# Kernel tuning notes

Hardware: AMD Instinct MI355X
Metric: run time of the kernel (lower is better)

Reference implementation:

```python
import jax, jax.numpy as jnp
import numpy as np

INPUT_DIM = 256
OUTPUT_DIM = 256
COND_DIM = 128
HIDDEN = 128
BATCH = 512


def setup_inputs() -> dict:
    key = jax.random.key(0)
    ks = jax.random.split(key, 8)
    IO = INPUT_DIM * OUTPUT_DIM
    x = jax.random.normal(ks[0], (BATCH, INPUT_DIM), dtype=jnp.float32)
    cond = jax.random.normal(ks[1], (BATCH, COND_DIM), dtype=jnp.float32)
    base_weight = jax.random.normal(ks[2], (INPUT_DIM, OUTPUT_DIM), dtype=jnp.float32) * 0.01
    base_bias = jnp.zeros((OUTPUT_DIM,), dtype=jnp.float32)
    # hypernet: Linear(cond_dim, hidden) -> ReLU -> Linear(hidden, I*O + O)
    w1 = jax.random.normal(ks[3], (COND_DIM, HIDDEN), dtype=jnp.float32) * (1.0 / np.sqrt(COND_DIM))
    b1 = jnp.zeros((HIDDEN,), dtype=jnp.float32)
    w2 = jax.random.normal(ks[4], (HIDDEN, IO + OUTPUT_DIM), dtype=jnp.float32) * (1.0 / np.sqrt(HIDDEN))
    b2 = jnp.zeros((IO + OUTPUT_DIM,), dtype=jnp.float32)
    return {"x": x, "cond": cond, "base_weight": base_weight, "base_bias": base_bias,
            "w1": w1, "b1": b1, "w2": w2, "b2": b2}


def reference(x, cond, base_weight, base_bias, w1, b1, w2, b2):
    B = x.shape[0]
    IO = INPUT_DIM * OUTPUT_DIM
    # hypernet MLP producing per-sample weight/bias deltas
    h = jax.nn.relu(cond @ w1 + b1)                      # [B, hidden]
    dyn = h @ w2 + b2                                    # [B, I*O + O]
    weight_delta = dyn[:, :IO].reshape(B, INPUT_DIM, OUTPUT_DIM)
    bias_delta = dyn[:, IO:]                             # [B, O]
    W = base_weight[None, :, :] + weight_delta           # [B, I, O]
    b = base_bias[None, :] + bias_delta                  # [B, O]
    out = jnp.einsum('bi,bio->bo', x, W) + b             # per-sample GEMV
    return out
```

## Files before the change

### kernel.cpp

```cpp
#include <hip/hip_runtime.h>
#include <hip/hip_bf16.h>
#include <stdint.h>

#define BATCH    512
#define IN_DIM   256
#define OUT_DIM  256
#define COND_DIM 128
#define HIDDEN   128
#define W2_COLS  65792
#define H_STRIDE 132
#define PLANE_SZ 65536
#define NCHUNKS  18
#define OUT_ELEMS (BATCH * OUT_DIM)
#define SLICE_OFF ((size_t)131 * PLANE_SZ)

typedef __attribute__((ext_vector_type(8))) short bf16x8;
typedef __attribute__((ext_vector_type(4))) float f32x4;

__device__ float          g_h[BATCH * H_STRIDE + 8];
__device__ unsigned short g_hbf[BATCH * HIDDEN];
__device__ unsigned short g_xbf[BATCH * IN_DIM];

static __device__ __forceinline__ unsigned short f2bf(float f) {
    union { float f; unsigned int u; } v; v.f = f;
    unsigned int r = v.u + 0x7FFFu + ((v.u >> 16) & 1u);
    return (unsigned short)(r >> 16);
}
static __device__ __forceinline__ unsigned int pack2(float a, float b) {
    return (unsigned int)f2bf(a) | ((unsigned int)f2bf(b) << 16);
}
static __device__ __forceinline__ float bf2f(unsigned short u) {
    union { unsigned int u; float f; } v; v.u = ((unsigned int)u) << 16;
    return v.f;
}

template<int N>
static __device__ __forceinline__ void wait_vmcnt() {
    if constexpr (N == 0)      asm volatile("s_waitcnt vmcnt(0)" ::: "memory");
    else if constexpr (N == 2) asm volatile("s_waitcnt vmcnt(2)" ::: "memory");
    else                       asm volatile("s_waitcnt vmcnt(4)" ::: "memory");
}

__global__ __launch_bounds__(256)
void hyper_prep_kernel(const float* __restrict__ x,
                       const float* __restrict__ cond,
                       const float* __restrict__ base_weight,
                       const float* __restrict__ w1,
                       const float* __restrict__ b1,
                       const float* __restrict__ w2,
                       const float* __restrict__ b2,
                       unsigned short* __restrict__ wt) {
    const int bx = blockIdx.x;
    const int t  = threadIdx.x;
    if (bx < 2088) {
        int p, it, ot; const float* src; int rstride;
        if (bx < 2080) {
            p = bx >> 4; int sub = bx & 15; it = sub >> 2; ot = sub & 3;
            src = (p < 128) ? (w2 + (size_t)p * W2_COLS) : (p == 128 ? b2 : base_weight);
            rstride = OUT_DIM;
        } else {
            p = 130; int sub = bx - 2080; it = sub >> 2; ot = sub & 3;
            src = w2 + 65536; rstride = W2_COLS;
        }
        int o  = ot * 64 + (t & 63);
        int i0 = it * 64 + (t >> 6) * 16;
        unsigned int vv[8];
        #pragma unroll
        for (int r = 0; r < 8; ++r) {
            float a = src[(size_t)(i0 + 2 * r)     * rstride + o];
            float b = src[(size_t)(i0 + 2 * r + 1) * rstride + o];
            vv[r] = pack2(a, b);
        }
        unsigned int* dst = (unsigned int*)(wt + (size_t)p * PLANE_SZ + (size_t)o * 256 + i0);
        *(uint4*)dst       = *(uint4*)&vv[0];
        *(uint4*)(dst + 4) = *(uint4*)&vv[4];
    } else if (bx < 2104) {
        int base = (bx - 2088) * 8192 + t * 32;
        #pragma unroll
        for (int g = 0; g < 4; ++g) {
            const float4* s4 = (const float4*)(x + base + g * 8);
            float4 a = s4[0], b = s4[1];
            unsigned int vv[4] = { pack2(a.x, a.y), pack2(a.z, a.w),
                                   pack2(b.x, b.y), pack2(b.z, b.w) };
            *(uint4*)(g_xbf + base + g * 8) = *(uint4*)vv;
        }
    } else {
        __shared__ float c[2][COND_DIM];
        int bb = t >> 7, k = t & 127;
        int b  = (bx - 2104) * 2 + bb;
        c[bb][k] = cond[b * COND_DIM + k];
        __syncthreads();
        float acc = b1[k];
        #pragma unroll 8
        for (int i = 0; i < COND_DIM; ++i)
            acc += c[bb][i] * w1[i * HIDDEN + k];
        acc = fmaxf(acc, 0.0f);
        g_h[b * H_STRIDE + k] = acc;
        g_hbf[b * HIDDEN + k] = f2bf(acc);
        if (k < 4) g_h[b * H_STRIDE + 128 + k] = 1.0f;
    }
}

template<int NSLABS>
static __device__ __forceinline__ void run_gemm(
    int nplanes, int p0, const unsigned short* asrc, int astride,
    const unsigned short* __restrict__ wt, unsigned short* __restrict__ slices,
    int chunk, int b0, int o0, int t,
    unsigned short (*B_lds)[64 * 64], const float* h_s)
{
    constexpr int LOG2S = (NSLABS == 4) ? 2 : 1;
    const int lane = t & 63, wave = t >> 6;
    const int wm = wave >> 1, wn = wave & 1;
    const int qg = lane >> 4, ncol = lane & 15;

    const int drow = lane >> 3;
    const int dcol = ((lane & 7) ^ drow) * 8;
    const int nsteps = nplanes * NSLABS;

    auto dmaB = [&](int s) {
        const int plane = p0 + (s >> LOG2S);
        const int i0    = (s & (NSLABS - 1)) * 64;
        const int buf   = s & 3;
        const unsigned short* gp = wt + (size_t)plane * PLANE_SZ
            + (size_t)(o0 + wave * 16 + drow) * 256 + i0 + dcol;
        __builtin_amdgcn_global_load_lds(
            (const __attribute__((address_space(1))) unsigned int*)gp,
            (__attribute__((address_space(3))) unsigned int*)&B_lds[buf][wave * 16 * 64],
            16, 0, 0);
        __builtin_amdgcn_global_load_lds(
            (const __attribute__((address_space(1))) unsigned int*)(gp + 8 * 256),
            (__attribute__((address_space(3))) unsigned int*)&B_lds[buf][(wave * 16 + 8) * 64],
            16, 0, 0);
    };

    bf16x8 xf[NSLABS][2][2];
    #pragma unroll
    for (int sl = 0; sl < NSLABS; ++sl)
        #pragma unroll
        for (int ks = 0; ks < 2; ++ks)
            #pragma unroll
            for (int mf = 0; mf < 2; ++mf)
                xf[sl][ks][mf] = *(const bf16x8*)(asrc
                    + (size_t)(b0 + wm * 32 + mf * 16 + ncol) * astride
                    + sl * 64 + ks * 32 + qg * 8);

    f32x4 acc[2][2] = {};
    f32x4 pacc[2][2];
    float hv[2][4];

    dmaB(0); dmaB(1);
    if (nsteps > 2) dmaB(2);

    for (int pl = 0; pl < nplanes; ++pl) {
        #pragma unroll
        for (int sl = 0; sl < NSLABS; ++sl) {
            const int s = pl * NSLABS + sl;

            if (s <= nsteps - 3)      wait_vmcnt<4>();
            else if (s == nsteps - 2) wait_vmcnt<2>();
            else                      wait_vmcnt<0>();
            __builtin_amdgcn_s_barrier();
            asm volatile("" ::: "memory");

            if (sl == 0) {
                #pragma unroll
                for (int mf = 0; mf < 2; ++mf)
                    #pragma unroll
                    for (int r = 0; r < 4; ++r)
                        hv[mf][r] = h_s[(wm * 32 + mf * 16 + qg * 4 + r) * 8 + pl];
                #pragma unroll
                for (int a = 0; a < 2; ++a)
                    #pragma unroll
                    for (int bq = 0; bq < 2; ++bq)
                        pacc[a][bq] = (f32x4){0.f, 0.f, 0.f, 0.f};
            }

            const int buf = s & 3;
            #pragma unroll
            for (int ks = 0; ks < 2; ++ks) {
                bf16x8 bfr[2];
                #pragma unroll
                for (int nf = 0; nf < 2; ++nf) {
                    int n = wn * 32 + nf * 16 + ncol;
                    bfr[nf] = *(const bf16x8*)&B_lds[buf][(n * 8 + ((ks * 4 + qg) ^ (n & 7))) * 8];
                }
                #pragma unroll
                for (int mf = 0; mf < 2; ++mf)
                    #pragma unroll
                    for (int nf = 0; nf < 2; ++nf)
                        pacc[mf][nf] = __builtin_amdgcn_mfma_f32_16x16x32_bf16(
                            xf[sl][ks][mf], bfr[nf], pacc[mf][nf], 0, 0, 0);
            }

            if (sl == NSLABS - 1) {
                #pragma unroll
                for (int mf = 0; mf < 2; ++mf)
                    #pragma unroll
                    for (int nf = 0; nf < 2; ++nf)
                        #pragma unroll
                        for (int r = 0; r < 4; ++r)
                            acc[mf][nf][r] += hv[mf][r] * pacc[mf][nf][r];
            }

            if (s + 3 < nsteps) dmaB(s + 3);
        }
    }

    unsigned short* slice = slices + (size_t)chunk * OUT_ELEMS;
    #pragma unroll
    for (int mf = 0; mf < 2; ++mf)
        #pragma unroll
        for (int nf = 0; nf < 2; ++nf)
            #pragma unroll
            for (int r = 0; r < 4; ++r) {
                int row = b0 + wm * 32 + mf * 16 + qg * 4 + r;
                int col = o0 + wn * 32 + nf * 16 + ncol;
                slice[(size_t)row * OUT_DIM + col] = f2bf(acc[mf][nf][r]);
            }
}

__global__ __launch_bounds__(256, 3)
void hyper_main_kernel(const unsigned short* __restrict__ wt,
                       unsigned short* __restrict__ slices) {
    __shared__ __align__(16) unsigned short B_lds[4][64 * 64];
    __shared__ float h_s[512];

    const int bx    = blockIdx.x;
    const int chunk = bx >> 5;
    const int rem   = bx & 31;
    const int b0    = (rem >> 2) * 64;
    const int o0    = (rem & 3) * 64;
    const int t     = threadIdx.x;

    const int p0 = (chunk < 16) ? chunk * 8 : (chunk == 16 ? 128 : 130);

    h_s[t]       = g_h[(b0      + (t >> 3)) * H_STRIDE + p0 + (t & 7)];
    h_s[256 + t] = g_h[(b0 + 32 + (t >> 3)) * H_STRIDE + p0 + (t & 7)];
    __syncthreads();

    if (chunk < 17)
        run_gemm<4>(chunk < 16 ? 8 : 2, p0, g_xbf, IN_DIM,
                    wt, slices, chunk, b0, o0, t, B_lds, h_s);
    else
        run_gemm<2>(1, p0, g_hbf, HIDDEN,
                    wt, slices, chunk, b0, o0, t, B_lds, h_s);
}

__global__ void hyper_reduce_kernel(const unsigned short* __restrict__ slices,
                                    const float* __restrict__ base_bias,
                                    const float* __restrict__ b2,
                                    float* __restrict__ out) {
    int i = blockIdx.x * 256 + threadIdx.x;
    int o = (i & 63) * 4;
    float4 bb = *(const float4*)(base_bias + o);
    float4 c2 = *(const float4*)(b2 + 65536 + o);
    float4 a;
    a.x = bb.x + c2.x; a.y = bb.y + c2.y; a.z = bb.z + c2.z; a.w = bb.w + c2.w;
    #pragma unroll
    for (int c = 0; c < NCHUNKS; ++c) {
        ushort4 v = *(const ushort4*)(slices + (size_t)c * OUT_ELEMS + (size_t)i * 4);
        a.x += bf2f(v.x); a.y += bf2f(v.y); a.z += bf2f(v.z); a.w += bf2f(v.w);
    }
    ((float4*)out)[i] = a;
}

extern "C" void kernel_launch(void* const* d_in, const int* in_sizes, int n_in,
                              void* d_out, int out_size, void* d_ws, size_t ws_size,
                              hipStream_t stream) {
    const float* x           = (const float*)d_in[0];
    const float* cond        = (const float*)d_in[1];
    const float* base_weight = (const float*)d_in[2];
    const float* base_bias   = (const float*)d_in[3];
    const float* w1          = (const float*)d_in[4];
    const float* b1          = (const float*)d_in[5];
    const float* w2          = (const float*)d_in[6];
    const float* b2          = (const float*)d_in[7];
    float* out = (float*)d_out;
    unsigned short* ws = (unsigned short*)d_ws;

    hyper_prep_kernel<<<2360, 256, 0, stream>>>(x, cond, base_weight, w1, b1, w2, b2, ws);
    hyper_main_kernel<<<NCHUNKS * 32, 256, 0, stream>>>(ws, ws + SLICE_OFF);
    hyper_reduce_kernel<<<OUT_ELEMS / 4 / 256, 256, 0, stream>>>(ws + SLICE_OFF, base_bias, b2, out);
}
```

Baseline: 120.1 us.

## Replace slice buffers and reduce kernel with atomic adds into output

Each main-kernel tile now atomically adds its fp32 partial sum straight into the output instead of writing a bf16 slice per chunk. The bias initialisation moves into extra blocks of the prep kernel, and the separate reduce kernel is removed. This drops one launch and the slice write/read traffic, and it also removes the bf16 rounding of partial sums. In exchange, 18 chunks contend through scattered scalar atomics, and the summation order is no longer deterministic.

```diff
diff --git a/kernel.cpp b/kernel.cpp
--- a/kernel.cpp
+++ b/kernel.cpp
@@ -12,7 +12,6 @@
 #define PLANE_SZ 65536
 #define NCHUNKS  18
 #define OUT_ELEMS (BATCH * OUT_DIM)
-#define SLICE_OFF ((size_t)131 * PLANE_SZ)
 
 typedef __attribute__((ext_vector_type(8))) short bf16x8;
 typedef __attribute__((ext_vector_type(4))) float f32x4;
@@ -28,10 +27,6 @@
 }
 static __device__ __forceinline__ unsigned int pack2(float a, float b) {
     return (unsigned int)f2bf(a) | ((unsigned int)f2bf(b) << 16);
-}
-static __device__ __forceinline__ float bf2f(unsigned short u) {
-    union { unsigned int u; float f; } v; v.u = ((unsigned int)u) << 16;
-    return v.f;
 }
 
 template<int N>
@@ -45,11 +40,13 @@
 void hyper_prep_kernel(const float* __restrict__ x,
                        const float* __restrict__ cond,
                        const float* __restrict__ base_weight,
+                       const float* __restrict__ base_bias,
                        const float* __restrict__ w1,
                        const float* __restrict__ b1,
                        const float* __restrict__ w2,
                        const float* __restrict__ b2,
-                       unsigned short* __restrict__ wt) {
+                       unsigned short* __restrict__ wt,
+                       float* __restrict__ out) {
     const int bx = blockIdx.x;
     const int t  = threadIdx.x;
     if (bx < 2088) {
@@ -84,7 +81,7 @@
                                    pack2(b.x, b.y), pack2(b.z, b.w) };
             *(uint4*)(g_xbf + base + g * 8) = *(uint4*)vv;
         }
-    } else {
+    } else if (bx < 2360) {
         __shared__ float c[2][COND_DIM];
         int bb = t >> 7, k = t & 127;
         int b  = (bx - 2104) * 2 + bb;
@@ -98,14 +95,22 @@
         g_h[b * H_STRIDE + k] = acc;
         g_hbf[b * HIDDEN + k] = f2bf(acc);
         if (k < 4) g_h[b * H_STRIDE + 128 + k] = 1.0f;
+    } else {
+        int i = (bx - 2360) * 256 + t;
+        int o = (i & 63) * 4;
+        float4 bb = *(const float4*)(base_bias + o);
+        float4 c2 = *(const float4*)(b2 + 65536 + o);
+        float4 a;
+        a.x = bb.x + c2.x; a.y = bb.y + c2.y; a.z = bb.z + c2.z; a.w = bb.w + c2.w;
+        ((float4*)out)[i] = a;
     }
 }
 
 template<int NSLABS>
 static __device__ __forceinline__ void run_gemm(
     int nplanes, int p0, const unsigned short* asrc, int astride,
-    const unsigned short* __restrict__ wt, unsigned short* __restrict__ slices,
-    int chunk, int b0, int o0, int t,
+    const unsigned short* __restrict__ wt, float* __restrict__ out,
+    int b0, int o0, int t,
     unsigned short (*B_lds)[64 * 64], const float* h_s)
 {
     constexpr int LOG2S = (NSLABS == 4) ? 2 : 1;
@@ -206,7 +211,6 @@
         }
     }
 
-    unsigned short* slice = slices + (size_t)chunk * OUT_ELEMS;
     #pragma unroll
     for (int mf = 0; mf < 2; ++mf)
         #pragma unroll
@@ -215,13 +219,13 @@
             for (int r = 0; r < 4; ++r) {
                 int row = b0 + wm * 32 + mf * 16 + qg * 4 + r;
                 int col = o0 + wn * 32 + nf * 16 + ncol;
-                slice[(size_t)row * OUT_DIM + col] = f2bf(acc[mf][nf][r]);
+                unsafeAtomicAdd(&out[(size_t)row * OUT_DIM + col], acc[mf][nf][r]);
             }
 }
 
 __global__ __launch_bounds__(256, 3)
 void hyper_main_kernel(const unsigned short* __restrict__ wt,
-                       unsigned short* __restrict__ slices) {
+                       float* __restrict__ out) {
     __shared__ __align__(16) unsigned short B_lds[4][64 * 64];
     __shared__ float h_s[512];
 
@@ -240,28 +244,10 @@
 
     if (chunk < 17)
         run_gemm<4>(chunk < 16 ? 8 : 2, p0, g_xbf, IN_DIM,
-                    wt, slices, chunk, b0, o0, t, B_lds, h_s);
+                    wt, out, b0, o0, t, B_lds, h_s);
     else
         run_gemm<2>(1, p0, g_hbf, HIDDEN,
-                    wt, slices, chunk, b0, o0, t, B_lds, h_s);
-}
-
-__global__ void hyper_reduce_kernel(const unsigned short* __restrict__ slices,
-                                    const float* __restrict__ base_bias,
-                                    const float* __restrict__ b2,
-                                    float* __restrict__ out) {
-    int i = blockIdx.x * 256 + threadIdx.x;
-    int o = (i & 63) * 4;
-    float4 bb = *(const float4*)(base_bias + o);
-    float4 c2 = *(const float4*)(b2 + 65536 + o);
-    float4 a;
-    a.x = bb.x + c2.x; a.y = bb.y + c2.y; a.z = bb.z + c2.z; a.w = bb.w + c2.w;
-    #pragma unroll
-    for (int c = 0; c < NCHUNKS; ++c) {
-        ushort4 v = *(const ushort4*)(slices + (size_t)c * OUT_ELEMS + (size_t)i * 4);
-        a.x += bf2f(v.x); a.y += bf2f(v.y); a.z += bf2f(v.z); a.w += bf2f(v.w);
-    }
-    ((float4*)out)[i] = a;
+                    wt, out, b0, o0, t, B_lds, h_s);
 }
 
 extern "C" void kernel_launch(void* const* d_in, const int* in_sizes, int n_in,
@@ -278,7 +264,7 @@
     float* out = (float*)d_out;
     unsigned short* ws = (unsigned short*)d_ws;
 
-    hyper_prep_kernel<<<2360, 256, 0, stream>>>(x, cond, base_weight, w1, b1, w2, b2, ws);
-    hyper_main_kernel<<<NCHUNKS * 32, 256, 0, stream>>>(ws, ws + SLICE_OFF);
-    hyper_reduce_kernel<<<OUT_ELEMS / 4 / 256, 256, 0, stream>>>(ws + SLICE_OFF, base_bias, b2, out);
-}
+    hyper_prep_kernel<<<2488, 256, 0, stream>>>(x, cond, base_weight, base_bias,
+                                                w1, b1, w2, b2, ws, out);
+    hyper_main_kernel<<<NCHUNKS * 32, 256, 0, stream>>>(ws, out);
+}
```

After: 121.2 us. Within noise of the previous version (+0.9%).
